# Kernel optimization log

Measured on AMD Instinct MI355X. Metric: run time of the kernel, lower is better.

The kernel has to match this reference:

```python
import jax, jax.numpy as jnp
import numpy as np

E = 8        # num_expert
D = 768      # d_model
H = 3072     # expert hidden = 4*d_model
K = 2        # top_k
N = 4096     # tokens
C = 2048


def setup_inputs() -> dict:
    key = jax.random.key(0)
    k0, k1, k2, k3 = jax.random.split(key, 4)
    moe_inp = jax.random.normal(k0, (N, D), dtype=jnp.float32)
    gate_w = jax.random.normal(k1, (D, E), dtype=jnp.float32) / np.sqrt(D).astype(np.float32)
    gate_b = jnp.zeros((E,), dtype=jnp.float32)
    w1 = jax.random.normal(k2, (E, D, H), dtype=jnp.float32) / np.sqrt(D).astype(np.float32)
    b1 = jnp.zeros((E, H), dtype=jnp.float32)
    w2 = jax.random.normal(k3, (E, H, D), dtype=jnp.float32) / np.sqrt(H).astype(np.float32)
    b2 = jnp.zeros((E, D), dtype=jnp.float32)
    return {"moe_inp": moe_inp, "gate_w": gate_w, "gate_b": gate_b,
            "w1": w1, "b1": b1, "w2": w2, "b2": b2}


def reference(moe_inp, gate_w, gate_b, w1, b1, w2, b2):
    # --- NaiveGate: linear scores, top-k experts, softmax over the k scores ---
    logits = moe_inp @ gate_w + gate_b                      # [N, E]
    top_v, top_i = jax.lax.top_k(logits, K)                 # [N, K]
    gate_score = jax.nn.softmax(top_v, axis=-1)             # [N, K]

    # --- scatter tokens to expert-contiguous capacity buffers (MOEScatter) ---
    flat_e = top_i.reshape(-1)                              # [N*K] expert id per slot
    onehot = jax.nn.one_hot(flat_e, E, dtype=jnp.int32)     # [N*K, E]
    # running position of each token inside its expert's buffer
    pos = jnp.sum(jnp.cumsum(onehot, axis=0) * onehot, axis=1) - 1  # [N*K]
    x_rep = jnp.repeat(moe_inp, K, axis=0)                  # [N*K, D]
    xe = jnp.zeros((E, C, D), dtype=moe_inp.dtype).at[flat_e, pos].set(x_rep, mode='drop')

    # --- grouped expert FFN (expert_fn): per-expert batched GEMMs ---
    h = jax.nn.gelu(jnp.einsum('ecd,edh->ech', xe, w1) + b1[:, None, :])
    ye = jnp.einsum('ech,ehd->ecd', h, w2) + b2[:, None, :]  # [E, C, D]

    # --- gather back to token order (MOEGather) and combine with gate scores ---
    y_flat = ye.at[flat_e, pos].get(mode='fill', fill_value=0.0)  # [N*K, D]
    out = jnp.einsum('nkd,nk->nd', y_flat.reshape(N, K, D), gate_score)
    return out
```

## Files before the change

### kernel.cpp

```cpp
#include <hip/hip_runtime.h>
#include <hip/hip_bf16.h>
#include <math.h>

#define NT    4096
#define DM    768
#define HD    3072
#define NE    8
#define CAP   2048
#define SLOTS_MAX 9216
#define WDIM2 40
#define BINCAP2 5

typedef __attribute__((ext_vector_type(8))) short bf16x8;
typedef __attribute__((ext_vector_type(4))) float f32x4;

__device__ __forceinline__ unsigned short f2bf(float f) {
  unsigned int u = __float_as_uint(f);
  unsigned int r = (u + 0x7fffu + ((u >> 16) & 1u)) >> 16;
  return (unsigned short)r;
}

__device__ __forceinline__ void async16(const unsigned short* g, unsigned short* l) {
  __builtin_amdgcn_global_load_lds((const __attribute__((address_space(1))) void*)g,
                                   (__attribute__((address_space(3))) void*)l,
                                   16, 0, 0);
}

__global__ void convert_x_kernel(const float* __restrict__ x,
                                 unsigned short* __restrict__ xb) {
  int i = (blockIdx.x * 256 + threadIdx.x) * 4;
  float4 v = *(const float4*)(x + i);
  uint2 o;
  o.x = (unsigned int)f2bf(v.x) | ((unsigned int)f2bf(v.y) << 16);
  o.y = (unsigned int)f2bf(v.z) | ((unsigned int)f2bf(v.w) << 16);
  *(uint2*)(xb + i) = o;
}

__global__ __launch_bounds__(256) void transpose_kernel(
    const float* __restrict__ src, unsigned short* __restrict__ dst,
    int R, int src_stride, int col_off,
    size_t src_e_stride, size_t dst_e_stride, int ncx) {
  __shared__ unsigned int tile32[64 * 129];
  const int b = blockIdx.x;
  const int e = b & 7;
  const int idx = b >> 3;
  const int c0 = (idx % ncx) * 64;
  const int r0 = (idx / ncx) * 256;
  const float* s = src + (size_t)e * src_e_stride + col_off;
  unsigned short* d = dst + (size_t)e * dst_e_stride;
  const int t = threadIdx.x;
  const int q16 = t & 15;
  const int tg = t >> 4;
#pragma unroll
  for (int i = 0; i < 8; i++) {
    int rl = tg * 2 + i * 32;
    const float4 f0 = *(const float4*)(s + (size_t)(r0 + rl) * src_stride + c0 + q16 * 4);
    const float4 f1 = *(const float4*)(s + (size_t)(r0 + rl + 1) * src_stride + c0 + q16 * 4);
    int j = tg + i * 16;
    tile32[(q16 * 4 + 0) * 129 + j] = (unsigned int)f2bf(f0.x) | ((unsigned int)f2bf(f1.x) << 16);
    tile32[(q16 * 4 + 1) * 129 + j] = (unsigned int)f2bf(f0.y) | ((unsigned int)f2bf(f1.y) << 16);
    tile32[(q16 * 4 + 2) * 129 + j] = (unsigned int)f2bf(f0.z) | ((unsigned int)f2bf(f1.z) << 16);
    tile32[(q16 * 4 + 3) * 129 + j] = (unsigned int)f2bf(f0.w) | ((unsigned int)f2bf(f1.w) << 16);
  }
  __syncthreads();
#pragma unroll
  for (int i = 0; i < 4; i++) {
    int cl = tg + i * 16;
    unsigned short* drow = d + (size_t)(c0 + cl) * R + r0;
#pragma unroll
    for (int half = 0; half < 2; half++) {
      int u = q16 * 4 + half * 64;
      uint4 v;
      v.x = tile32[cl * 129 + u + 0];
      v.y = tile32[cl * 129 + u + 1];
      v.z = tile32[cl * 129 + u + 2];
      v.w = tile32[cl * 129 + u + 3];
      *(uint4*)(drow + q16 * 8 + half * 128) = v;
    }
  }
}

__global__ void gate_dots_kernel(const float* __restrict__ inp,
                                 const float* __restrict__ gw,
                                 const float* __restrict__ gb,
                                 int2* __restrict__ tope,
                                 float2* __restrict__ tops) {
  const int tok  = blockIdx.x * 4 + (threadIdx.x >> 6);
  const int lane = threadIdx.x & 63;
  const float* x = inp + (size_t)tok * DM;
  float acc[NE];
#pragma unroll
  for (int e = 0; e < NE; e++) acc[e] = 0.f;
  for (int d = lane; d < DM; d += 64) {
    float xv = x[d];
    const float4 w0 = *(const float4*)(gw + d * NE);
    const float4 w1v = *(const float4*)(gw + d * NE + 4);
    acc[0] += xv * w0.x; acc[1] += xv * w0.y;
    acc[2] += xv * w0.z; acc[3] += xv * w0.w;
    acc[4] += xv * w1v.x; acc[5] += xv * w1v.y;
    acc[6] += xv * w1v.z; acc[7] += xv * w1v.w;
  }
#pragma unroll
  for (int e = 0; e < NE; e++) {
    float v = acc[e];
#pragma unroll
    for (int m = 32; m > 0; m >>= 1) v += __shfl_xor(v, m, 64);
    acc[e] = v + gb[e];
  }
  if (lane == 0) {
    float bv = -1e30f, sv = -1e30f; int bi = 0, si = 0;
#pragma unroll
    for (int e = 0; e < NE; e++) {
      float v = acc[e];
      if (v > bv)      { sv = bv; si = bi; bv = v; bi = e; }
      else if (v > sv) { sv = v;  si = e; }
    }
    float e1 = expf(sv - bv);
    float s0 = 1.f / (1.f + e1);
    float s1 = e1 / (1.f + e1);
    tope[tok] = make_int2(bi, si);
    tops[tok] = make_float2(s0, s1);
  }
}

__device__ __forceinline__ int agg_inc(int* lcnt, int key) {
  const int lane = threadIdx.x & 63;
  int p = 0;
#pragma unroll
  for (int ee = 0; ee < NE; ee++) {
    unsigned long long m = __ballot(key == ee);
    if (m) {
      int leader = __ffsll(m) - 1;
      int n = __popcll(m);
      int b = 0;
      if (lane == leader) b = atomicAdd(&lcnt[ee], n);
      b = __shfl(b, leader, 64);
      if (key == ee) p = b + __popcll(m & ((1ull << lane) - 1ull));
    }
  }
  return p;
}

__global__ void assign_kernel(const int2* __restrict__ tope,
                              int* __restrict__ cnt,
                              int* __restrict__ base,
                              int* __restrict__ src,
                              int2* __restrict__ pos,
                              int2* __restrict__ wl) {
  __shared__ int lcnt[NE];
  const int t = threadIdx.x;
  if (t < NE) lcnt[t] = 0;
  __syncthreads();
  for (int i = t; i < NT; i += 1024) {
    int2 e = tope[i];
    int p0 = agg_inc(lcnt, e.x);
    int p1 = agg_inc(lcnt, e.y);
    if (p0 < CAP) src[e.x * CAP + p0] = i;
    if (p1 < CAP) src[e.y * CAP + p1] = i;
    pos[i] = make_int2(p0, p1);
  }
  __syncthreads();
  if (t == 0) {
    int b = 0;
    for (int e = 0; e < NE; e++) {
      int c = min(lcnt[e], CAP);
      cnt[e] = c;
      base[e] = b;
      b += (c + 127) & ~127;
    }
    for (int s = 0; s < WDIM2; s++) wl[s] = make_int2(-1, 0);
    int bin = 0, fill = 0;
    for (int e = 0; e < NE; e++) {
      int ntl = (cnt[e] + 255) >> 8;
      for (int mt = 0; mt < ntl; mt++) {
        if (fill == BINCAP2) { bin++; fill = 0; }
        wl[fill * 8 + bin] = make_int2(e, mt * 256);
        fill++;
      }
    }
  }
}

__global__ __launch_bounds__(512) void gemm1_kernel(
    const unsigned short* __restrict__ xb,
    const unsigned short* __restrict__ w1t,
    const float* __restrict__ b1,
    const int* __restrict__ cnt,
    const int* __restrict__ base,
    const int* __restrict__ src,
    const int2* __restrict__ wl,
    unsigned short* __restrict__ h,
    int hoff, int chunk) {
  const int b = blockIdx.x;
  const int wi = b % WDIM2;
  const int nt = b / WDIM2;
  const int2 wle = wl[wi];
  if (wle.x < 0) return;
  const int e = wle.x;
  const int m0 = wle.y;
  const int n0 = nt * 256;
  const int count = cnt[e];
  const int cpad = (count + 127) & ~127;
  const int hb = base[e];

  __shared__ unsigned short As[3 * 8192];
  __shared__ unsigned short Bs[3 * 8192];

  const int t = threadIdx.x;
  const int lane = t & 63;
  const int wave = t >> 6;
  const int r0 = t >> 2;
  const int kc = ((t & 3) ^ ((t >> 3) & 3)) * 8;

  const int tok0 = (m0 + r0       < count) ? src[e * CAP + m0 + r0]       : 0;
  const int tok1 = (m0 + r0 + 128 < count) ? src[e * CAP + m0 + r0 + 128] : 0;
  const unsigned short* aptr0 = xb + (size_t)tok0 * DM + kc;
  const unsigned short* aptr1 = xb + (size_t)tok1 * DM + kc;
  const unsigned short* w1e = w1t + (size_t)e * chunk * DM;
  const unsigned short* bptr0 = w1e + (size_t)(n0 + r0) * DM + kc;
  const unsigned short* bptr1 = bptr0 + (size_t)128 * DM;

  const int wrow = (wave >> 2) * 128;
  const int wcol = (wave & 3) * 64;
  const int lrow = lane & 15;
  const int koff = ((lane >> 4) ^ ((lane >> 1) & 3)) * 8;

  f32x4 acc[8][4];
#pragma unroll
  for (int i = 0; i < 8; i++)
#pragma unroll
    for (int j = 0; j < 4; j++) acc[i][j] = (f32x4){0.f, 0.f, 0.f, 0.f};

#define STAGE1(bi, kk) do {                                   \
    unsigned short* A_ = As + (bi) * 8192 + wave * 512;       \
    unsigned short* B_ = Bs + (bi) * 8192 + wave * 512;       \
    async16(aptr0 + (kk), A_);                                \
    async16(aptr1 + (kk), A_ + 4096);                         \
    async16(bptr0 + (kk), B_);                                \
    async16(bptr1 + (kk), B_ + 4096);                         \
  } while (0)

#define COMPUTE1(bi) do {                                               \
    const unsigned short* A_ = As + (bi) * 8192;                        \
    const unsigned short* B_ = Bs + (bi) * 8192;                        \
    bf16x8 af[8], bfr[4];                                               \
    _Pragma("unroll")                                                   \
    for (int i = 0; i < 8; i++)                                         \
      af[i] = *(const bf16x8*)(A_ + (wrow + i * 16 + lrow) * 32 + koff);\
    _Pragma("unroll")                                                   \
    for (int j = 0; j < 4; j++)                                         \
      bfr[j] = *(const bf16x8*)(B_ + (wcol + j * 16 + lrow) * 32 + koff);\
    _Pragma("unroll")                                                   \
    for (int i = 0; i < 8; i++)                                         \
      _Pragma("unroll")                                                 \
      for (int j = 0; j < 4; j++)                                       \
        acc[i][j] = __builtin_amdgcn_mfma_f32_16x16x32_bf16(af[i], bfr[j], acc[i][j], 0, 0, 0); \
  } while (0)

  const int NS = DM / 32;
  STAGE1(0, 0);
  STAGE1(1, 32);
  int cur = 0;
  for (int ts = 0; ts < NS - 2; ++ts) {
    int pf = cur + 2; if (pf >= 3) pf -= 3;
    STAGE1(pf, (ts + 2) * 32);
    asm volatile("s_waitcnt vmcnt(8)" ::: "memory");
    __builtin_amdgcn_s_barrier();
    COMPUTE1(cur);
    asm volatile("s_waitcnt lgkmcnt(0)" ::: "memory");
    __builtin_amdgcn_s_barrier();
    if (++cur == 3) cur = 0;
  }
  asm volatile("s_waitcnt vmcnt(4)" ::: "memory");
  __builtin_amdgcn_s_barrier();
  COMPUTE1(cur);
  if (++cur == 3) cur = 0;
  asm volatile("s_waitcnt vmcnt(0)" ::: "memory");
  __builtin_amdgcn_s_barrier();
  COMPUTE1(cur);

  const int q4 = (lane >> 4) * 4;
  const int c = lane & 15;
  unsigned short* hrow = h + (size_t)(hb + m0) * chunk + n0;
#pragma unroll
  for (int j = 0; j < 4; j++) {
    const float bias = b1[e * HD + hoff + n0 + wcol + j * 16 + c];
#pragma unroll
    for (int i = 0; i < 8; i++) {
#pragma unroll
      for (int r = 0; r < 4; r++) {
        int m = wrow + i * 16 + q4 + r;
        if (m0 + m < cpad) {
          float v = acc[i][j][r] + bias;
          float u2 = 1.5957691216f * (v + 0.044715f * v * v * v);
          float g = v / (1.f + __expf(-u2));
          hrow[(size_t)m * chunk + wcol + j * 16 + c] = f2bf(g);
        }
      }
    }
  }
#undef STAGE1
#undef COMPUTE1
}

__global__ __launch_bounds__(512) void gemm2_kernel(
    const unsigned short* __restrict__ h,
    const unsigned short* __restrict__ w2t,
    const int* __restrict__ cnt,
    const int* __restrict__ base,
    const int2* __restrict__ wl,
    float* __restrict__ ye,
    int chunk, int add_prev) {
  const int b = blockIdx.x;
  const int wi = b % WDIM2;
  const int fast = b / WDIM2;
  const int2 wle = wl[wi];
  if (wle.x < 0) return;
  const int e = wle.x;
  const int m0 = wle.y;
  const int kh = fast / 3;
  const int n0 = (fast % 3) * 256;
  const int count = cnt[e];
  const int cpad = (count + 127) & ~127;
  const int hb = base[e];
  const int khalf = chunk >> 1;

  __shared__ unsigned short As[3 * 8192];
  __shared__ unsigned short Bs[3 * 8192];

  const int t = threadIdx.x;
  const int lane = t & 63;
  const int wave = t >> 6;
  const int r0 = t >> 2;
  const int kc = ((t & 3) ^ ((t >> 3) & 3)) * 8;

  const unsigned short* aptr0 = h + (size_t)(hb + m0 + r0) * chunk + kh * khalf + kc;
  const unsigned short* aptr1 = aptr0 + (size_t)128 * chunk;
  const unsigned short* w2e = w2t + (size_t)e * DM * chunk;
  const unsigned short* bptr0 = w2e + (size_t)(n0 + r0) * chunk + kh * khalf + kc;
  const unsigned short* bptr1 = bptr0 + (size_t)128 * chunk;

  const int wrow = (wave >> 2) * 128;
  const int wcol = (wave & 3) * 64;
  const int lrow = lane & 15;
  const int koff = ((lane >> 4) ^ ((lane >> 1) & 3)) * 8;

  f32x4 acc[8][4];
#pragma unroll
  for (int i = 0; i < 8; i++)
#pragma unroll
    for (int j = 0; j < 4; j++) acc[i][j] = (f32x4){0.f, 0.f, 0.f, 0.f};

#define STAGE2(bi, kk) do {                                   \
    unsigned short* A_ = As + (bi) * 8192 + wave * 512;       \
    unsigned short* B_ = Bs + (bi) * 8192 + wave * 512;       \
    async16(aptr0 + (kk), A_);                                \
    async16(aptr1 + (kk), A_ + 4096);                         \
    async16(bptr0 + (kk), B_);                                \
    async16(bptr1 + (kk), B_ + 4096);                         \
  } while (0)

#define COMPUTE2(bi) do {                                               \
    const unsigned short* A_ = As + (bi) * 8192;                        \
    const unsigned short* B_ = Bs + (bi) * 8192;                        \
    bf16x8 af[8], bfr[4];                                               \
    _Pragma("unroll")                                                   \
    for (int i = 0; i < 8; i++)                                         \
      af[i] = *(const bf16x8*)(A_ + (wrow + i * 16 + lrow) * 32 + koff);\
    _Pragma("unroll")                                                   \
    for (int j = 0; j < 4; j++)                                         \
      bfr[j] = *(const bf16x8*)(B_ + (wcol + j * 16 + lrow) * 32 + koff);\
    _Pragma("unroll")                                                   \
    for (int i = 0; i < 8; i++)                                         \
      _Pragma("unroll")                                                 \
      for (int j = 0; j < 4; j++)                                       \
        acc[i][j] = __builtin_amdgcn_mfma_f32_16x16x32_bf16(af[i], bfr[j], acc[i][j], 0, 0, 0); \
  } while (0)

  const int NS = khalf >> 5;
  STAGE2(0, 0);
  STAGE2(1, 32);
  int cur = 0;
  for (int ts = 0; ts < NS - 2; ++ts) {
    int pf = cur + 2; if (pf >= 3) pf -= 3;
    STAGE2(pf, (ts + 2) * 32);
    asm volatile("s_waitcnt vmcnt(8)" ::: "memory");
    __builtin_amdgcn_s_barrier();
    COMPUTE2(cur);
    asm volatile("s_waitcnt lgkmcnt(0)" ::: "memory");
    __builtin_amdgcn_s_barrier();
    if (++cur == 3) cur = 0;
  }
  asm volatile("s_waitcnt vmcnt(4)" ::: "memory");
  __builtin_amdgcn_s_barrier();
  COMPUTE2(cur);
  if (++cur == 3) cur = 0;
  asm volatile("s_waitcnt vmcnt(0)" ::: "memory");
  __builtin_amdgcn_s_barrier();
  COMPUTE2(cur);

  const int q4 = (lane >> 4) * 4;
  const int c = lane & 15;
  float* yrow = ye + (size_t)kh * SLOTS_MAX * DM + (size_t)(hb + m0) * DM + n0;
#pragma unroll
  for (int i = 0; i < 8; i++) {
#pragma unroll
    for (int r = 0; r < 4; r++) {
      int m = wrow + i * 16 + q4 + r;
      if (m0 + m < cpad) {
#pragma unroll
        for (int j = 0; j < 4; j++) {
          int n = wcol + j * 16 + c;
          float v = acc[i][j][r];
          if (add_prev) v += yrow[(size_t)m * DM + n];
          yrow[(size_t)m * DM + n] = v;
        }
      }
    }
  }
#undef STAGE2
#undef COMPUTE2
}

__global__ void gather_kernel(const float* __restrict__ ye,
                              const float* __restrict__ b2,
                              const int2* __restrict__ tope,
                              const float2* __restrict__ tops,
                              const int2* __restrict__ pos,
                              const int* __restrict__ base,
                              float* __restrict__ out) {
  int idx = blockIdx.x * 256 + threadIdx.x;
  int tok = idx / (DM / 4);
  int d4 = (idx % (DM / 4)) * 4;
  int2 e = tope[tok];
  float2 s = tops[tok];
  int2 p = pos[tok];
  const float* ye1 = ye + (size_t)SLOTS_MAX * DM;
  float4 r = make_float4(0.f, 0.f, 0.f, 0.f);
  if (p.x < CAP) {
    size_t row = (size_t)(base[e.x] + p.x) * DM + d4;
    const float4 va = *(const float4*)(ye + row);
    const float4 vb = *(const float4*)(ye1 + row);
    const float4 bb = *(const float4*)(b2 + e.x * DM + d4);
    r.x += s.x * (va.x + vb.x + bb.x); r.y += s.x * (va.y + vb.y + bb.y);
    r.z += s.x * (va.z + vb.z + bb.z); r.w += s.x * (va.w + vb.w + bb.w);
  }
  if (p.y < CAP) {
    size_t row = (size_t)(base[e.y] + p.y) * DM + d4;
    const float4 va = *(const float4*)(ye + row);
    const float4 vb = *(const float4*)(ye1 + row);
    const float4 bb = *(const float4*)(b2 + e.y * DM + d4);
    r.x += s.y * (va.x + vb.x + bb.x); r.y += s.y * (va.y + vb.y + bb.y);
    r.z += s.y * (va.z + vb.z + bb.z); r.w += s.y * (va.w + vb.w + bb.w);
  }
  *(float4*)(out + (size_t)tok * DM + d4) = r;
}

extern "C" void kernel_launch(void* const* d_in, const int* in_sizes, int n_in,
                              void* d_out, int out_size, void* d_ws, size_t ws_size,
                              hipStream_t stream) {
  const float* inp = (const float*)d_in[0];
  const float* gw  = (const float*)d_in[1];
  const float* gb  = (const float*)d_in[2];
  const float* w1  = (const float*)d_in[3];
  const float* b1  = (const float*)d_in[4];
  const float* w2  = (const float*)d_in[5];
  const float* b2  = (const float*)d_in[6];
  float* out = (float*)d_out;

  const size_t meta = 165376;
  const int cands[6] = {3072, 1536, 1024, 768, 512, 256};
  int chunk = 256;
  for (int ci = 0; ci < 6; ci++) {
    int c = cands[ci];
    size_t need = meta + (size_t)NT * DM * 2
                + (size_t)NE * c * DM * 2
                + (size_t)SLOTS_MAX * c * 2
                + 2 * (size_t)SLOTS_MAX * DM * 4;
    if (need <= ws_size) { chunk = c; break; }
  }

  char* ws = (char*)d_ws;
  int*    cnt  = (int*)(ws);
  int*    base = (int*)(ws + 256);
  int*    srcb = (int*)(ws + 512);
  int2*   tope = (int2*)(ws + 66048);
  float2* tops = (float2*)(ws + 98816);
  int2*   pos  = (int2*)(ws + 131584);
  int2*   wl   = (int2*)(ws + 164352);
  size_t off = meta;
  unsigned short* xb = (unsigned short*)(ws + off);  off += (size_t)NT * DM * 2;
  unsigned short* wt = (unsigned short*)(ws + off);  off += (size_t)NE * chunk * DM * 2;
  unsigned short* hc = (unsigned short*)(ws + off);  off += (size_t)SLOTS_MAX * chunk * 2;
  float* ye = (float*)(ws + off);

  convert_x_kernel<<<(NT * DM) / 1024, 256, 0, stream>>>(inp, xb);
  gate_dots_kernel<<<NT / 4, 256, 0, stream>>>(inp, gw, gb, tope, tops);
  assign_kernel<<<1, 1024, 0, stream>>>(tope, cnt, base, srcb, pos, wl);

  for (int c = 0; c < HD; c += chunk) {
    transpose_kernel<<<NE * (chunk / 64) * (DM / 256), 256, 0, stream>>>(
        w1, wt, DM, HD, c, (size_t)DM * HD, (size_t)chunk * DM, chunk / 64);
    gemm1_kernel<<<(chunk / 256) * WDIM2, 512, 0, stream>>>(
        xb, wt, b1, cnt, base, srcb, wl, hc, c, chunk);
    transpose_kernel<<<NE * (DM / 64) * (chunk / 256), 256, 0, stream>>>(
        w2 + (size_t)c * DM, wt, chunk, DM, 0, (size_t)HD * DM, (size_t)DM * chunk, DM / 64);
    gemm2_kernel<<<(2 * DM / 256) * WDIM2, 512, 0, stream>>>(
        hc, wt, cnt, base, wl, ye, chunk, c == 0 ? 0 : 1);
  }

  gather_kernel<<<(NT * DM / 4) / 256, 256, 0, stream>>>(ye, b2, tope, tops, pos, base, out);
}
```

Baseline: 409.2 us.

## Shrink gemm1 tiles to 128x128 with own worklist and LDS-staged stores

gemm1 now uses 128x128 output tiles with 256 threads instead of 256x256 with 512, and gets its own worklist (72 slots, 128-row m-tiles) built in assign_kernel, separate from gemm2's. The GELU epilogue writes bf16 results into reused LDS slabs and then copies them to global memory as 16-byte vector rows instead of scattered 2-byte stores. The aim is more blocks for better CU occupancy and load balance across uneven expert counts, plus coalesced output writes. In exchange each loaded tile gets less reuse, and the cpad row guard is dropped because all 128-row tiles now fit inside the padded region.

```diff
diff --git a/kernel.cpp b/kernel.cpp
--- a/kernel.cpp
+++ b/kernel.cpp
@@ -8,6 +8,8 @@
 #define NE    8
 #define CAP   2048
 #define SLOTS_MAX 9216
+#define WDIM1 72
+#define BINCAP1 9
 #define WDIM2 40
 #define BINCAP2 5
 
@@ -146,7 +148,8 @@
                               int* __restrict__ base,
                               int* __restrict__ src,
                               int2* __restrict__ pos,
-                              int2* __restrict__ wl) {
+                              int2* __restrict__ wl1,
+                              int2* __restrict__ wl2) {
   __shared__ int lcnt[NE];
   const int t = threadIdx.x;
   if (t < NE) lcnt[t] = 0;
@@ -168,20 +171,30 @@
       base[e] = b;
       b += (c + 127) & ~127;
     }
-    for (int s = 0; s < WDIM2; s++) wl[s] = make_int2(-1, 0);
+    for (int s = 0; s < WDIM1; s++) wl1[s] = make_int2(-1, 0);
     int bin = 0, fill = 0;
+    for (int e = 0; e < NE; e++) {
+      int ntl = (cnt[e] + 127) >> 7;
+      for (int mt = 0; mt < ntl; mt++) {
+        if (fill == BINCAP1) { bin++; fill = 0; }
+        wl1[fill * 8 + bin] = make_int2(e, mt * 128);
+        fill++;
+      }
+    }
+    for (int s = 0; s < WDIM2; s++) wl2[s] = make_int2(-1, 0);
+    bin = 0; fill = 0;
     for (int e = 0; e < NE; e++) {
       int ntl = (cnt[e] + 255) >> 8;
       for (int mt = 0; mt < ntl; mt++) {
         if (fill == BINCAP2) { bin++; fill = 0; }
-        wl[fill * 8 + bin] = make_int2(e, mt * 256);
+        wl2[fill * 8 + bin] = make_int2(e, mt * 256);
         fill++;
       }
     }
   }
 }
 
-__global__ __launch_bounds__(512) void gemm1_kernel(
+__global__ __launch_bounds__(256) void gemm1_kernel(
     const unsigned short* __restrict__ xb,
     const unsigned short* __restrict__ w1t,
     const float* __restrict__ b1,
@@ -192,19 +205,18 @@
     unsigned short* __restrict__ h,
     int hoff, int chunk) {
   const int b = blockIdx.x;
-  const int wi = b % WDIM2;
-  const int nt = b / WDIM2;
+  const int wi = b % WDIM1;
+  const int nt = b / WDIM1;
   const int2 wle = wl[wi];
   if (wle.x < 0) return;
   const int e = wle.x;
   const int m0 = wle.y;
-  const int n0 = nt * 256;
+  const int n0 = nt * 128;
   const int count = cnt[e];
-  const int cpad = (count + 127) & ~127;
   const int hb = base[e];
 
-  __shared__ unsigned short As[3 * 8192];
-  __shared__ unsigned short Bs[3 * 8192];
+  __shared__ unsigned short As[3 * 4096];
+  __shared__ unsigned short Bs[3 * 4096];
 
   const int t = threadIdx.x;
   const int lane = t & 63;
@@ -212,46 +224,46 @@
   const int r0 = t >> 2;
   const int kc = ((t & 3) ^ ((t >> 3) & 3)) * 8;
 
-  const int tok0 = (m0 + r0       < count) ? src[e * CAP + m0 + r0]       : 0;
-  const int tok1 = (m0 + r0 + 128 < count) ? src[e * CAP + m0 + r0 + 128] : 0;
+  const int tok0 = (m0 + r0      < count) ? src[e * CAP + m0 + r0]      : 0;
+  const int tok1 = (m0 + r0 + 64 < count) ? src[e * CAP + m0 + r0 + 64] : 0;
   const unsigned short* aptr0 = xb + (size_t)tok0 * DM + kc;
   const unsigned short* aptr1 = xb + (size_t)tok1 * DM + kc;
   const unsigned short* w1e = w1t + (size_t)e * chunk * DM;
   const unsigned short* bptr0 = w1e + (size_t)(n0 + r0) * DM + kc;
-  const unsigned short* bptr1 = bptr0 + (size_t)128 * DM;
-
-  const int wrow = (wave >> 2) * 128;
-  const int wcol = (wave & 3) * 64;
+  const unsigned short* bptr1 = bptr0 + (size_t)64 * DM;
+
+  const int wrow = (wave >> 1) * 64;
+  const int wcol = (wave & 1) * 64;
   const int lrow = lane & 15;
   const int koff = ((lane >> 4) ^ ((lane >> 1) & 3)) * 8;
 
-  f32x4 acc[8][4];
-#pragma unroll
-  for (int i = 0; i < 8; i++)
+  f32x4 acc[4][4];
+#pragma unroll
+  for (int i = 0; i < 4; i++)
 #pragma unroll
     for (int j = 0; j < 4; j++) acc[i][j] = (f32x4){0.f, 0.f, 0.f, 0.f};
 
 #define STAGE1(bi, kk) do {                                   \
-    unsigned short* A_ = As + (bi) * 8192 + wave * 512;       \
-    unsigned short* B_ = Bs + (bi) * 8192 + wave * 512;       \
+    unsigned short* A_ = As + (bi) * 4096 + wave * 512;       \
+    unsigned short* B_ = Bs + (bi) * 4096 + wave * 512;       \
     async16(aptr0 + (kk), A_);                                \
-    async16(aptr1 + (kk), A_ + 4096);                         \
+    async16(aptr1 + (kk), A_ + 2048);                         \
     async16(bptr0 + (kk), B_);                                \
-    async16(bptr1 + (kk), B_ + 4096);                         \
+    async16(bptr1 + (kk), B_ + 2048);                         \
   } while (0)
 
 #define COMPUTE1(bi) do {                                               \
-    const unsigned short* A_ = As + (bi) * 8192;                        \
-    const unsigned short* B_ = Bs + (bi) * 8192;                        \
-    bf16x8 af[8], bfr[4];                                               \
+    const unsigned short* A_ = As + (bi) * 4096;                        \
+    const unsigned short* B_ = Bs + (bi) * 4096;                        \
+    bf16x8 af[4], bfr[4];                                               \
     _Pragma("unroll")                                                   \
-    for (int i = 0; i < 8; i++)                                         \
+    for (int i = 0; i < 4; i++)                                         \
       af[i] = *(const bf16x8*)(A_ + (wrow + i * 16 + lrow) * 32 + koff);\
     _Pragma("unroll")                                                   \
     for (int j = 0; j < 4; j++)                                         \
       bfr[j] = *(const bf16x8*)(B_ + (wcol + j * 16 + lrow) * 32 + koff);\
     _Pragma("unroll")                                                   \
-    for (int i = 0; i < 8; i++)                                         \
+    for (int i = 0; i < 4; i++)                                         \
       _Pragma("unroll")                                                 \
       for (int j = 0; j < 4; j++)                                       \
         acc[i][j] = __builtin_amdgcn_mfma_f32_16x16x32_bf16(af[i], bfr[j], acc[i][j], 0, 0, 0); \
@@ -279,25 +291,33 @@
   __builtin_amdgcn_s_barrier();
   COMPUTE1(cur);
 
+  __syncthreads();
   const int q4 = (lane >> 4) * 4;
   const int c = lane & 15;
-  unsigned short* hrow = h + (size_t)(hb + m0) * chunk + n0;
+  unsigned short* slab = (wave < 2) ? (As + wave * 4608) : (Bs + (wave - 2) * 4608);
 #pragma unroll
   for (int j = 0; j < 4; j++) {
     const float bias = b1[e * HD + hoff + n0 + wcol + j * 16 + c];
 #pragma unroll
-    for (int i = 0; i < 8; i++) {
+    for (int i = 0; i < 4; i++) {
 #pragma unroll
       for (int r = 0; r < 4; r++) {
-        int m = wrow + i * 16 + q4 + r;
-        if (m0 + m < cpad) {
-          float v = acc[i][j][r] + bias;
-          float u2 = 1.5957691216f * (v + 0.044715f * v * v * v);
-          float g = v / (1.f + __expf(-u2));
-          hrow[(size_t)m * chunk + wcol + j * 16 + c] = f2bf(g);
-        }
+        float v = acc[i][j][r] + bias;
+        float u2 = 1.5957691216f * (v + 0.044715f * v * v * v);
+        float g = v / (1.f + __expf(-u2));
+        slab[(i * 16 + q4 + r) * 72 + j * 16 + c] = f2bf(g);
       }
     }
+  }
+  asm volatile("s_waitcnt lgkmcnt(0)" ::: "memory");
+  const int l8 = lane & 7;
+  const int r8 = lane >> 3;
+  unsigned short* hrow = h + (size_t)(hb + m0 + wrow) * chunk + n0 + wcol;
+#pragma unroll
+  for (int p = 0; p < 8; p++) {
+    int lm = p * 8 + r8;
+    uint4 v = *(const uint4*)(slab + lm * 72 + l8 * 8);
+    *(uint4*)(hrow + (size_t)lm * chunk + l8 * 8) = v;
   }
 #undef STAGE1
 #undef COMPUTE1
@@ -487,7 +507,8 @@
   int2*   tope = (int2*)(ws + 66048);
   float2* tops = (float2*)(ws + 98816);
   int2*   pos  = (int2*)(ws + 131584);
-  int2*   wl   = (int2*)(ws + 164352);
+  int2*   wl1  = (int2*)(ws + 164352);
+  int2*   wl2  = (int2*)(ws + 164928);
   size_t off = meta;
   unsigned short* xb = (unsigned short*)(ws + off);  off += (size_t)NT * DM * 2;
   unsigned short* wt = (unsigned short*)(ws + off);  off += (size_t)NE * chunk * DM * 2;
@@ -496,17 +517,17 @@
 
   convert_x_kernel<<<(NT * DM) / 1024, 256, 0, stream>>>(inp, xb);
   gate_dots_kernel<<<NT / 4, 256, 0, stream>>>(inp, gw, gb, tope, tops);
-  assign_kernel<<<1, 1024, 0, stream>>>(tope, cnt, base, srcb, pos, wl);
+  assign_kernel<<<1, 1024, 0, stream>>>(tope, cnt, base, srcb, pos, wl1, wl2);
 
   for (int c = 0; c < HD; c += chunk) {
     transpose_kernel<<<NE * (chunk / 64) * (DM / 256), 256, 0, stream>>>(
         w1, wt, DM, HD, c, (size_t)DM * HD, (size_t)chunk * DM, chunk / 64);
-    gemm1_kernel<<<(chunk / 256) * WDIM2, 512, 0, stream>>>(
-        xb, wt, b1, cnt, base, srcb, wl, hc, c, chunk);
+    gemm1_kernel<<<(chunk / 128) * WDIM1, 256, 0, stream>>>(
+        xb, wt, b1, cnt, base, srcb, wl1, hc, c, chunk);
     transpose_kernel<<<NE * (DM / 64) * (chunk / 256), 256, 0, stream>>>(
         w2 + (size_t)c * DM, wt, chunk, DM, 0, (size_t)HD * DM, (size_t)DM * chunk, DM / 64);
     gemm2_kernel<<<(2 * DM / 256) * WDIM2, 512, 0, stream>>>(
-        hc, wt, cnt, base, wl, ye, chunk, c == 0 ? 0 : 1);
+        hc, wt, cnt, base, wl2, ye, chunk, c == 0 ? 0 : 1);
   }
 
   gather_kernel<<<(NT * DM / 4) / 256, 256, 0, stream>>>(ye, b2, tope, tops, pos, base, out);
```

New measurement: 382.0 us. -6.7%, faster.
